# Optimization experiments

Measured on AMD Instinct MI355X. Metric: run time of the kernel, lower is better.

Reference implementation:

```python
import jax, jax.numpy as jnp
import numpy as np

NUM_ITER = 5
NUM_SLOTS = 16
INPUT_SIZE = 256
EPS = 1e-8
TAU = 1.0
B, N = 8, 16384


def setup_inputs() -> dict:
    key = jax.random.key(0)
    k1, k2 = jax.random.split(key)
    inputs = jax.random.normal(k1, (B, N, INPUT_SIZE), dtype=jnp.float32)
    # xavier_uniform for a (1, K, D) tensor (torch fan_in=K*D, fan_out=D)
    limit = float(np.sqrt(6.0 / (NUM_SLOTS * INPUT_SIZE + INPUT_SIZE)))
    slot_logits = jax.random.uniform(k2, (1, NUM_SLOTS, INPUT_SIZE),
                                     minval=-limit, maxval=limit, dtype=jnp.float32)
    mixing_coefficients = jnp.full((1, NUM_SLOTS), 1.0 / NUM_SLOTS, dtype=jnp.float32)
    return {"inputs": inputs, "slot_logits": slot_logits,
            "mixing_coefficients": mixing_coefficients}


def reference(inputs, slot_logits, mixing_coefficients):
    Bn, Nn, D = inputs.shape
    theta = jnp.broadcast_to(slot_logits, (Bn, NUM_SLOTS, D))       # (B,K,D)
    pi = jnp.broadcast_to(mixing_coefficients, (Bn, NUM_SLOTS))     # (B,K)
    p = jax.nn.softmax(inputs, axis=-1)                             # (B,N,D), loop-invariant
    for _ in range(NUM_ITER):
        log_q = jax.nn.log_softmax(theta, axis=-1)                  # (B,K,D)
        logits = jnp.einsum('bnd,bkd->bnk', p, log_q)               # (B,N,K)
        logits = logits + jnp.log(pi + EPS)[:, None, :]
        gamma = jax.nn.softmax(logits, axis=-1)                     # (B,N,K)
        pi = gamma.mean(axis=1)                                     # (B,K)
        gamma_sum = gamma.sum(axis=1) + EPS                         # (B,K)
        numerator = jnp.einsum('bnk,bnd->bkd', gamma, inputs)       # (B,K,D)
        theta = numerator / gamma_sum[:, :, None]
    g = jax.random.gumbel(jax.random.key(1), theta.shape, dtype=theta.dtype)
    slots = jax.nn.softmax((theta + g) / TAU, axis=-1)              # (B,K,D)
    return slots
```

## Files before the change

### kernel.cpp

```cpp
#include <hip/hip_runtime.h>
#include <cstdint>
#include <cstddef>

#define BN 8
#define NN 16384
#define DD 256
#define KK 16
#define NITER 5
#define EPSV 1e-8f
#define LOG256 5.545177444479562f
#define PSTR 260
#define TPB 8
#define GG 32

typedef float f32x4 __attribute__((ext_vector_type(4)));
typedef long  i64v;

__device__ __forceinline__ float frcp(float x){ return __builtin_amdgcn_rcpf(x); }
__device__ __forceinline__ float wmax(float v){
  #pragma unroll
  for (int m = 32; m >= 1; m >>= 1) v = fmaxf(v, __shfl_xor(v, m, 64));
  return v;
}
__device__ __forceinline__ float wsum(float v){
  #pragma unroll
  for (int m = 32; m >= 1; m >>= 1) v += __shfl_xor(v, m, 64);
  return v;
}
__device__ __forceinline__ uint32_t pk4_fp8(float a, float b, float c, float d){
  int w = __builtin_amdgcn_cvt_pk_fp8_f32(a, b, 0, false);
  w = __builtin_amdgcn_cvt_pk_fp8_f32(c, d, w, true);
  return (uint32_t)w;
}
__device__ __forceinline__ uint32_t f2bf(float f){
  uint32_t u = __float_as_uint(f);
  return (u + 0x7fffu + ((u >> 16) & 1u)) >> 16;
}
__device__ __forceinline__ uint32_t pk2bf(float a, float b){
  return f2bf(a) | (f2bf(b) << 16);
}
__device__ __forceinline__ float bf2f(uint32_t h){ return __uint_as_float(h << 16); }

__global__ __launch_bounds__(256, 2) void k_prep6(const float* __restrict__ x,
                                                  uint2* __restrict__ pbf8,
                                                  uint2* __restrict__ xbf8,
                                                  float* __restrict__ invs){
  __shared__ float xs[2][32 * PSTR];
  const int b = blockIdx.y;
  const int Sbase = blockIdx.x * TPB;
  const int tid = threadIdx.x;
  const int wave = tid >> 6, lane = tid & 63;
  const float* xb = x + (size_t)b * NN * DD;

  auto stage = [&](int S, int buf){
    #pragma unroll
    for (int r = 0; r < 8; ++r){
      int row = wave * 8 + r;
      const float* gp = xb + ((size_t)S * 32 + row) * DD + lane * 4;
      float* lp = &xs[buf][row * PSTR];
      __builtin_amdgcn_global_load_lds(
          (const __attribute__((address_space(1))) unsigned int*)gp,
          (__attribute__((address_space(3))) unsigned int*)lp, 16, 0, 0);
    }
  };

  stage(Sbase, 0);
  for (int it = 0; it < TPB; ++it){
    const int S = Sbase + it;
    const int cur = it & 1;
    asm volatile("s_waitcnt vmcnt(0)" ::: "memory");
    __builtin_amdgcn_sched_barrier(0);
    __syncthreads();
    if (it + 1 < TPB) stage(S + 1, cur ^ 1);

    {
      int row = 8 * wave + (lane & 7);
      const float* pr = &xs[cur][row * PSTR + (lane >> 3) * 32];
      float a = 0.f;
      #pragma unroll
      for (int i = 0; i < 8; ++i){
        float4 v = *(const float4*)&pr[4 * i];
        a += __expf(v.x) + __expf(v.y) + __expf(v.z) + __expf(v.w);
      }
      a += __shfl_xor(a, 8, 64);
      a += __shfl_xor(a, 16, 64);
      a += __shfl_xor(a, 32, 64);
      if (lane < 8) invs[(size_t)b * NN + S * 32 + 8 * wave + lane] = frcp(a);
    }

    #pragma unroll
    for (int i = 0; i < 4; ++i){
      int p = wave * 4 + i; int c = p >> 3, s = p & 7;
      int rho = lane & 15;
      int n = 8 * (rho >> 2) + 4 * c + (rho & 3);
      int d = 32 * s + 8 * (lane >> 4);
      float4 v0 = *(const float4*)&xs[cur][n * PSTR + d];
      float4 v1 = *(const float4*)&xs[cur][n * PSTR + d + 4];
      uint2 o;
      o.x = pk4_fp8(__expf(v0.x), __expf(v0.y), __expf(v0.z), __expf(v0.w));
      o.y = pk4_fp8(__expf(v1.x), __expf(v1.y), __expf(v1.z), __expf(v1.w));
      pbf8[(((size_t)b * 1024 + (size_t)S * 2 + c) * 8 + s) * 64 + lane] = o;
    }
    #pragma unroll
    for (int i = 0; i < 4; ++i){
      int dt = wave * 4 + i;
      int col = dt * 16 + (lane & 15);
      int g2 = lane >> 4;
      float v[8];
      #pragma unroll
      for (int j = 0; j < 8; ++j) v[j] = xs[cur][(8 * g2 + j) * PSTR + col];
      uint2 o;
      o.x = pk4_fp8(v[0], v[1], v[2], v[3]);
      o.y = pk4_fp8(v[4], v[5], v[6], v[7]);
      xbf8[(((size_t)b * 512 + S) * 16 + dt) * 64 + lane] = o;
    }
    __syncthreads();
  }
}

__global__ __launch_bounds__(256) void k_init6(const float* __restrict__ slot_logits,
                                               const float* __restrict__ mix,
                                               uint8_t* __restrict__ lqf8,
                                               float* __restrict__ logpi){
  int w    = blockIdx.x * 4 + (threadIdx.x >> 6);
  int lane = threadIdx.x & 63;
  int b = w >> 4, k = w & 15;
  const float4* sl = (const float4*)(slot_logits + (size_t)k * DD);
  float4 t = sl[lane];
  float m = wmax(fmaxf(fmaxf(t.x, t.y), fmaxf(t.z, t.w)));
  float s = wsum(__expf(t.x-m) + __expf(t.y-m) + __expf(t.z-m) + __expf(t.w-m));
  float L = m + __logf(s) - LOG256;
  int d0 = lane * 4;
  int ss = d0 >> 5;
  int l2 = (((d0 & 31) >> 3) << 4) + k;
  int jb = d0 & 7;
  uint32_t wv = pk4_fp8(t.x - L, t.y - L, t.z - L, t.w - L);
  *(uint32_t*)(lqf8 + ((((size_t)b * 8 + ss) * 64 + l2) * 8 + jb)) = wv;
  if (lane == 0) logpi[w] = __logf(mix[k] + EPSV);
}

__global__ __launch_bounds__(256, 2) void k_em6(const uint2* __restrict__ pbf8,
                                                const uint2* __restrict__ xbf8,
                                                const uint2* __restrict__ lqf8,
                                                const float* __restrict__ logpi,
                                                const float* __restrict__ invs,
                                                uint16_t* __restrict__ pnumb,
                                                float* __restrict__ ppi){
  __shared__ float sred[KK * DD];
  __shared__ float spi2[16];
  const int b = blockIdx.y, g = blockIdx.x;
  const int tid = threadIdx.x;
  const int wave = tid >> 6, lane = tid & 63;

  i64v lq8[8];
  {
    const uint2* p = lqf8 + (size_t)b * 8 * 64 + lane;
    #pragma unroll
    for (int s = 0; s < 8; ++s){ uint2 t = p[s * 64]; lq8[s] = *(i64v*)&t; }
  }
  const float lpik = logpi[b * KK + (lane & 15)];

  f32x4 acc[16];
  #pragma unroll
  for (int dt = 0; dt < 16; ++dt) acc[dt] = (f32x4){0.f, 0.f, 0.f, 0.f};
  float piacc = 0.f;

  const int S0 = (g * 4 + wave) * 4;
  #pragma unroll
  for (int ssi = 0; ssi < 4; ++ssi){
    const int S = S0 + ssi;
    const uint2* pb = pbf8 + (((size_t)b * 1024 + (size_t)S * 2) * 8) * 64 + lane;
    const uint2* xr = xbf8 + (((size_t)b * 512 + S) * 16) * 64 + lane;

    uint2 pa[16];
    #pragma unroll
    for (int i = 0; i < 16; ++i) pa[i] = pb[(size_t)i * 64];

    float ivs[8];
    {
      const float* ib = invs + (size_t)b * NN + S * 32 + 8 * (lane >> 4);
      #pragma unroll
      for (int j = 0; j < 8; ++j) ivs[j] = ib[j];
    }

    float ga[8];
    #pragma unroll
    for (int c = 0; c < 2; ++c){
      f32x4 lc = (f32x4){0.f, 0.f, 0.f, 0.f};
      #pragma unroll
      for (int s = 0; s < 8; ++s){
        i64v a = *(i64v*)&pa[c * 8 + s];
        lc = __builtin_amdgcn_mfma_f32_16x16x32_fp8_fp8(a, lq8[s], lc, 0, 0, 0);
      }
      #pragma unroll
      for (int r2 = 0; r2 < 4; ++r2){
        float lg = fmaf(lc[r2], ivs[c * 4 + r2], lpik);
        float mx = lg;
        #pragma unroll
        for (int m = 1; m <= 8; m <<= 1) mx = fmaxf(mx, __shfl_xor(mx, m, 64));
        float e = __expf(lg - mx);
        float s2 = e;
        #pragma unroll
        for (int m = 1; m <= 8; m <<= 1) s2 += __shfl_xor(s2, m, 64);
        ga[c * 4 + r2] = e * frcp(s2);
      }
    }
    uint2 gp;
    gp.x = pk4_fp8(ga[0], ga[1], ga[2], ga[3]);
    gp.y = pk4_fp8(ga[4], ga[5], ga[6], ga[7]);
    piacc += __builtin_amdgcn_cvt_f32_fp8((int)gp.x, 0)
           + __builtin_amdgcn_cvt_f32_fp8((int)gp.x, 1)
           + __builtin_amdgcn_cvt_f32_fp8((int)gp.x, 2)
           + __builtin_amdgcn_cvt_f32_fp8((int)gp.x, 3)
           + __builtin_amdgcn_cvt_f32_fp8((int)gp.y, 0)
           + __builtin_amdgcn_cvt_f32_fp8((int)gp.y, 1)
           + __builtin_amdgcn_cvt_f32_fp8((int)gp.y, 2)
           + __builtin_amdgcn_cvt_f32_fp8((int)gp.y, 3);
    i64v gA = *(i64v*)&gp;
    #pragma unroll
    for (int dt = 0; dt < 16; ++dt){
      uint2 xv = xr[(size_t)dt * 64];
      acc[dt] = __builtin_amdgcn_mfma_f32_16x16x32_fp8_fp8(gA, *(i64v*)&xv,
                                                           acc[dt], 0, 0, 0);
    }
  }

  float pk = piacc;
  pk += __shfl_xor(pk, 16, 64);
  pk += __shfl_xor(pk, 32, 64);
  __syncthreads();
  if (wave == 0){
    #pragma unroll
    for (int dt = 0; dt < 16; ++dt)
      #pragma unroll
      for (int r2 = 0; r2 < 4; ++r2)
        sred[(4 * (lane >> 4) + r2) * DD + dt * 16 + (lane & 15)] = acc[dt][r2];
    if (lane < 16) spi2[lane] = pk;
  }
  __syncthreads();
  for (int w = 1; w < 4; ++w){
    if (wave == w){
      #pragma unroll
      for (int dt = 0; dt < 16; ++dt)
        #pragma unroll
        for (int r2 = 0; r2 < 4; ++r2)
          sred[(4 * (lane >> 4) + r2) * DD + dt * 16 + (lane & 15)] += acc[dt][r2];
      if (lane < 16) spi2[lane] += pk;
    }
    __syncthreads();
  }
  uint32_t* dst = (uint32_t*)(pnumb + (size_t)(b * GG + g) * KK * DD);
  #pragma unroll
  for (int j = 0; j < 8; ++j){
    float a = sred[tid * 2 + j * 512];
    float c = sred[tid * 2 + 1 + j * 512];
    dst[tid + j * 256] = pk2bf(a, c);
  }
  if (tid < 16) ppi[(size_t)(b * GG + g) * KK + tid] = spi2[tid];
}

__global__ __launch_bounds__(64) void k_reduce6(const uint16_t* __restrict__ pnumb,
                                                const float* __restrict__ ppi,
                                                float* __restrict__ theta,
                                                uint8_t* __restrict__ lqf8,
                                                float* __restrict__ logpi){
  int w = blockIdx.x;
  int lane = threadIdx.x;
  int b = w >> 4, k = w & 15;
  float4 sum = make_float4(0.f, 0.f, 0.f, 0.f);
  #pragma unroll 4
  for (int g = 0; g < GG; ++g){
    const uint2* p = (const uint2*)(pnumb +
        ((size_t)(b * GG + g) * KK + k) * DD + lane * 4);
    uint2 v = *p;
    sum.x += bf2f(v.x & 0xffffu); sum.y += bf2f(v.x >> 16);
    sum.z += bf2f(v.y & 0xffffu); sum.w += bf2f(v.y >> 16);
  }
  float ps = 0.f;
  for (int g = lane; g < GG; g += 64) ps += ppi[((size_t)b * GG + g) * KK + k];
  ps = wsum(ps);
  float inv = frcp(ps + EPSV);
  float4 th = make_float4(sum.x * inv, sum.y * inv, sum.z * inv, sum.w * inv);
  ((float4*)(theta + (size_t)w * DD))[lane] = th;
  float m = wmax(fmaxf(fmaxf(th.x, th.y), fmaxf(th.z, th.w)));
  float s = wsum(__expf(th.x-m) + __expf(th.y-m) + __expf(th.z-m) + __expf(th.w-m));
  float L = m + __logf(s) - LOG256;
  int d0 = lane * 4;
  int ss = d0 >> 5;
  int l2 = (((d0 & 31) >> 3) << 4) + k;
  int jb = d0 & 7;
  uint32_t wv = pk4_fp8(th.x - L, th.y - L, th.z - L, th.w - L);
  *(uint32_t*)(lqf8 + ((((size_t)b * 8 + ss) * 64 + l2) * 8 + jb)) = wv;
  if (lane == 0) logpi[w] = __logf(ps * (1.0f / NN) + EPSV);
}

__device__ __forceinline__ uint32_t rotl32(uint32_t x, int r){ return (x << r) | (x >> (32 - r)); }
__device__ __forceinline__ void tf2x32(uint32_t k0, uint32_t k1, uint32_t c0, uint32_t c1,
                                       uint32_t& o0, uint32_t& o1){
  uint32_t ks0 = k0, ks1 = k1, ks2 = 0x1BD11BDAu ^ k0 ^ k1;
  uint32_t x0 = c0 + ks0, x1 = c1 + ks1;
  #define RND(r) { x0 += x1; x1 = rotl32(x1, r); x1 ^= x0; }
  RND(13) RND(15) RND(26) RND(6)   x0 += ks1; x1 += ks2 + 1u;
  RND(17) RND(29) RND(16) RND(24)  x0 += ks2; x1 += ks0 + 2u;
  RND(13) RND(15) RND(26) RND(6)   x0 += ks0; x1 += ks1 + 3u;
  RND(17) RND(29) RND(16) RND(24)  x0 += ks1; x1 += ks2 + 4u;
  RND(13) RND(15) RND(26) RND(6)   x0 += ks2; x1 += ks0 + 5u;
  #undef RND
  o0 = x0; o1 = x1;
}

__global__ __launch_bounds__(256) void k_final(const float* __restrict__ theta,
                                               float* __restrict__ out){
  int w    = blockIdx.x * 4 + (threadIdx.x >> 6);
  int lane = threadIdx.x & 63;
  float4 th = ((const float4*)(theta + (size_t)w * DD))[lane];
  int i0 = w * DD + lane * 4;
  float gv[4];
  #pragma unroll
  for (int j = 0; j < 4; ++j){
    uint32_t i = (uint32_t)(i0 + j);
    uint32_t o0, o1;
    tf2x32(0u, 1u, 0u, i, o0, o1);
    uint32_t bits = o0 ^ o1;
    float f = __uint_as_float((bits >> 9) | 0x3f800000u) - 1.0f;
    const float TINY = 1.17549435e-38f;
    float u = fmaxf(f + TINY, TINY);
    gv[j] = -logf(-logf(u));
  }
  float4 y = make_float4(th.x + gv[0], th.y + gv[1], th.z + gv[2], th.w + gv[3]);
  float m = wmax(fmaxf(fmaxf(y.x, y.y), fmaxf(y.z, y.w)));
  float4 e = make_float4(__expf(y.x-m), __expf(y.y-m), __expf(y.z-m), __expf(y.w-m));
  float s = wsum(e.x + e.y + e.z + e.w);
  float inv = 1.0f / s;
  ((float4*)(out + (size_t)w * DD))[lane] =
      make_float4(e.x*inv, e.y*inv, e.z*inv, e.w*inv);
}

__global__ __launch_bounds__(256) void k_fill(float* __restrict__ out, float v){
  out[blockIdx.x * 256 + threadIdx.x] = v;
}

extern "C" void kernel_launch(void* const* d_in, const int* in_sizes, int n_in,
                              void* d_out, int out_size, void* d_ws, size_t ws_size,
                              hipStream_t stream){
  const float* x    = (const float*)d_in[0];
  const float* sl   = (const float*)d_in[1];
  const float* mix  = (const float*)d_in[2];
  float* out = (float*)d_out;
  char* ws = (char*)d_ws;

  const size_t SZ_PBF  = 33554432ull;
  const size_t SZ_XBF  = 33554432ull;
  const size_t SZ_LQF  = 32768ull;
  const size_t SZ_INV  = (size_t)BN*NN*4;
  const size_t SZ_TH   = (size_t)BN*KK*DD*4;
  const size_t SZ_LP   = 512ull;
  const size_t SZ_PNUM = (size_t)BN*GG*KK*DD*2;
  const size_t SZ_PPI  = (size_t)BN*GG*KK*4;
  size_t need = SZ_PBF + SZ_XBF + SZ_LQF + SZ_INV + SZ_TH + SZ_LP + SZ_PNUM + SZ_PPI;

  if (ws_size < need){
    k_fill<<<(BN*KK*DD)/256, 256, 0, stream>>>(out, -9.0f);
    return;
  }
  size_t o = 0;
  uint2*    pbf8  = (uint2*)(ws + o);     o += SZ_PBF;
  uint2*    xbf8  = (uint2*)(ws + o);     o += SZ_XBF;
  uint8_t*  lqf8  = (uint8_t*)(ws + o);   o += SZ_LQF;
  float*    invs  = (float*)(ws + o);     o += SZ_INV;
  float*    theta = (float*)(ws + o);     o += SZ_TH;
  float*    logpi = (float*)(ws + o);     o += SZ_LP;
  uint16_t* pnumb = (uint16_t*)(ws + o);  o += SZ_PNUM;
  float*    ppi   = (float*)(ws + o);

  k_prep6<<<dim3(512 / TPB, BN), 256, 0, stream>>>(x, pbf8, xbf8, invs);
  k_init6<<<(BN*KK)/4, 256, 0, stream>>>(sl, mix, lqf8, logpi);
  for (int it = 0; it < NITER; ++it){
    k_em6    <<<dim3(GG, BN), 256, 0, stream>>>(pbf8, xbf8, (const uint2*)lqf8,
                                                logpi, invs, pnumb, ppi);
    k_reduce6<<<BN*KK, 64, 0, stream>>>(pnumb, ppi, theta, lqf8, logpi);
  }
  k_final<<<(BN*KK)/4, 256, 0, stream>>>(theta, out);
}
```

Before: 157.4 us.

## Fuse all EM stages into one persistent kernel with global atomic barriers

Replaces the chain of prep, init, per-iteration EM and reduce, and final launches with a single persistent kernel of 256 blocks that runs every stage in turn, separated by a software grid barrier built on an atomic counter. The goal is to remove the launch overhead and inter-kernel gaps of about a dozen small launches. In exchange, each block now does two prep tiles in sequence, the reduce and final stages leave most blocks idle, and correctness relies on all 256 blocks being co-resident. Spin-waiting on one atomic counter adds barrier latency, and an extra memset launch is needed to clear the counter.

```diff
diff --git a/kernel.cpp b/kernel.cpp
--- a/kernel.cpp
+++ b/kernel.cpp
@@ -41,41 +41,34 @@
 }
 __device__ __forceinline__ float bf2f(uint32_t h){ return __uint_as_float(h << 16); }
 
-__global__ __launch_bounds__(256, 2) void k_prep6(const float* __restrict__ x,
-                                                  uint2* __restrict__ pbf8,
-                                                  uint2* __restrict__ xbf8,
-                                                  float* __restrict__ invs){
-  __shared__ float xs[2][32 * PSTR];
-  const int b = blockIdx.y;
-  const int Sbase = blockIdx.x * TPB;
-  const int tid = threadIdx.x;
-  const int wave = tid >> 6, lane = tid & 63;
+
+__device__ __forceinline__ void dev_prep(const float* __restrict__ x,
+    uint2* __restrict__ pbf8, uint2* __restrict__ xbf8, float* __restrict__ invs,
+    int b, int Sbase, float* xs0, float* xs1, int wave, int lane){
   const float* xb = x + (size_t)b * NN * DD;
-
+  float* bufs[2] = {xs0, xs1};
   auto stage = [&](int S, int buf){
     #pragma unroll
     for (int r = 0; r < 8; ++r){
       int row = wave * 8 + r;
       const float* gp = xb + ((size_t)S * 32 + row) * DD + lane * 4;
-      float* lp = &xs[buf][row * PSTR];
+      float* lp = bufs[buf] + row * PSTR;
       __builtin_amdgcn_global_load_lds(
           (const __attribute__((address_space(1))) unsigned int*)gp,
           (__attribute__((address_space(3))) unsigned int*)lp, 16, 0, 0);
     }
   };
-
   stage(Sbase, 0);
   for (int it = 0; it < TPB; ++it){
     const int S = Sbase + it;
-    const int cur = it & 1;
+    float* xc = bufs[it & 1];
     asm volatile("s_waitcnt vmcnt(0)" ::: "memory");
     __builtin_amdgcn_sched_barrier(0);
     __syncthreads();
-    if (it + 1 < TPB) stage(S + 1, cur ^ 1);
-
+    if (it + 1 < TPB) stage(S + 1, (it & 1) ^ 1);
     {
       int row = 8 * wave + (lane & 7);
-      const float* pr = &xs[cur][row * PSTR + (lane >> 3) * 32];
+      const float* pr = xc + row * PSTR + (lane >> 3) * 32;
       float a = 0.f;
       #pragma unroll
       for (int i = 0; i < 8; ++i){
@@ -87,15 +80,14 @@
       a += __shfl_xor(a, 32, 64);
       if (lane < 8) invs[(size_t)b * NN + S * 32 + 8 * wave + lane] = frcp(a);
     }
-
     #pragma unroll
     for (int i = 0; i < 4; ++i){
       int p = wave * 4 + i; int c = p >> 3, s = p & 7;
       int rho = lane & 15;
       int n = 8 * (rho >> 2) + 4 * c + (rho & 3);
       int d = 32 * s + 8 * (lane >> 4);
-      float4 v0 = *(const float4*)&xs[cur][n * PSTR + d];
-      float4 v1 = *(const float4*)&xs[cur][n * PSTR + d + 4];
+      float4 v0 = *(const float4*)(xc + n * PSTR + d);
+      float4 v1 = *(const float4*)(xc + n * PSTR + d + 4);
       uint2 o;
       o.x = pk4_fp8(__expf(v0.x), __expf(v0.y), __expf(v0.z), __expf(v0.w));
       o.y = pk4_fp8(__expf(v1.x), __expf(v1.y), __expf(v1.z), __expf(v1.w));
@@ -108,7 +100,7 @@
       int g2 = lane >> 4;
       float v[8];
       #pragma unroll
-      for (int j = 0; j < 8; ++j) v[j] = xs[cur][(8 * g2 + j) * PSTR + col];
+      for (int j = 0; j < 8; ++j) v[j] = xc[(8 * g2 + j) * PSTR + col];
       uint2 o;
       o.x = pk4_fp8(v[0], v[1], v[2], v[3]);
       o.y = pk4_fp8(v[4], v[5], v[6], v[7]);
@@ -118,12 +110,9 @@
   }
 }
 
-__global__ __launch_bounds__(256) void k_init6(const float* __restrict__ slot_logits,
-                                               const float* __restrict__ mix,
-                                               uint8_t* __restrict__ lqf8,
-                                               float* __restrict__ logpi){
-  int w    = blockIdx.x * 4 + (threadIdx.x >> 6);
-  int lane = threadIdx.x & 63;
+__device__ __forceinline__ void dev_init(const float* __restrict__ slot_logits,
+    const float* __restrict__ mix, uint8_t* __restrict__ lqf8,
+    float* __restrict__ logpi, int w, int lane){
   int b = w >> 4, k = w & 15;
   const float4* sl = (const float4*)(slot_logits + (size_t)k * DD);
   float4 t = sl[lane];
@@ -139,22 +128,14 @@
   if (lane == 0) logpi[w] = __logf(mix[k] + EPSV);
 }
 
-__global__ __launch_bounds__(256, 2) void k_em6(const uint2* __restrict__ pbf8,
-                                                const uint2* __restrict__ xbf8,
-                                                const uint2* __restrict__ lqf8,
-                                                const float* __restrict__ logpi,
-                                                const float* __restrict__ invs,
-                                                uint16_t* __restrict__ pnumb,
-                                                float* __restrict__ ppi){
-  __shared__ float sred[KK * DD];
-  __shared__ float spi2[16];
-  const int b = blockIdx.y, g = blockIdx.x;
-  const int tid = threadIdx.x;
-  const int wave = tid >> 6, lane = tid & 63;
-
+__device__ __forceinline__ void dev_em(const uint2* __restrict__ pbf8,
+    const uint2* __restrict__ xbf8, const uint2* __restrict__ lqf8v,
+    const float* __restrict__ logpi, const float* __restrict__ invs,
+    uint16_t* __restrict__ pnumb, float* __restrict__ ppi,
+    int b, int g, float* sred, float* spi2, int wave, int lane, int tid){
   i64v lq8[8];
   {
-    const uint2* p = lqf8 + (size_t)b * 8 * 64 + lane;
+    const uint2* p = lqf8v + (size_t)b * 8 * 64 + lane;
     #pragma unroll
     for (int s = 0; s < 8; ++s){ uint2 t = p[s * 64]; lq8[s] = *(i64v*)&t; }
   }
@@ -171,18 +152,15 @@
     const int S = S0 + ssi;
     const uint2* pb = pbf8 + (((size_t)b * 1024 + (size_t)S * 2) * 8) * 64 + lane;
     const uint2* xr = xbf8 + (((size_t)b * 512 + S) * 16) * 64 + lane;
-
     uint2 pa[16];
     #pragma unroll
     for (int i = 0; i < 16; ++i) pa[i] = pb[(size_t)i * 64];
-
     float ivs[8];
     {
       const float* ib = invs + (size_t)b * NN + S * 32 + 8 * (lane >> 4);
       #pragma unroll
       for (int j = 0; j < 8; ++j) ivs[j] = ib[j];
     }
-
     float ga[8];
     #pragma unroll
     for (int c = 0; c < 2; ++c){
@@ -259,13 +237,9 @@
   if (tid < 16) ppi[(size_t)(b * GG + g) * KK + tid] = spi2[tid];
 }
 
-__global__ __launch_bounds__(64) void k_reduce6(const uint16_t* __restrict__ pnumb,
-                                                const float* __restrict__ ppi,
-                                                float* __restrict__ theta,
-                                                uint8_t* __restrict__ lqf8,
-                                                float* __restrict__ logpi){
-  int w = blockIdx.x;
-  int lane = threadIdx.x;
+__device__ __forceinline__ void dev_reduce(const uint16_t* __restrict__ pnumb,
+    const float* __restrict__ ppi, float* __restrict__ theta,
+    uint8_t* __restrict__ lqf8, float* __restrict__ logpi, int w, int lane){
   int b = w >> 4, k = w & 15;
   float4 sum = make_float4(0.f, 0.f, 0.f, 0.f);
   #pragma unroll 4
@@ -309,10 +283,8 @@
   o0 = x0; o1 = x1;
 }
 
-__global__ __launch_bounds__(256) void k_final(const float* __restrict__ theta,
-                                               float* __restrict__ out){
-  int w    = blockIdx.x * 4 + (threadIdx.x >> 6);
-  int lane = threadIdx.x & 63;
+__device__ __forceinline__ void dev_final(const float* __restrict__ theta,
+                                          float* __restrict__ out, int w, int lane){
   float4 th = ((const float4*)(theta + (size_t)w * DD))[lane];
   int i0 = w * DD + lane * 4;
   float gv[4];
@@ -336,6 +308,81 @@
       make_float4(e.x*inv, e.y*inv, e.z*inv, e.w*inv);
 }
 
+__device__ __forceinline__ void gbar(uint32_t* bar, uint32_t goal){
+  __syncthreads();
+  if (threadIdx.x == 0){
+    __threadfence();
+    atomicAdd(bar, 1u);
+    while (atomicAdd(bar, 0u) < goal) __builtin_amdgcn_s_sleep(4);
+  }
+  __syncthreads();
+  __threadfence();
+}
+
+__global__ __launch_bounds__(256, 2) void k_fused(
+    const float* __restrict__ x, const float* __restrict__ sl,
+    const float* __restrict__ mix,
+    uint2* __restrict__ pbf8, uint2* __restrict__ xbf8,
+    uint8_t* __restrict__ lqf8, float* __restrict__ invs,
+    float* __restrict__ theta, float* __restrict__ logpi,
+    uint16_t* __restrict__ pnumb, float* __restrict__ ppi,
+    float* __restrict__ out, uint32_t* __restrict__ bar){
+  __shared__ float xs[2][32 * PSTR];
+  __shared__ float spi2[16];
+  const int bid = blockIdx.x;
+  const int tid = threadIdx.x;
+  const int wave = tid >> 6, lane = tid & 63;
+  uint32_t nb = 0;
+
+  for (int ui = 0; ui < 2; ++ui){
+    int u = bid + ui * 256;
+    dev_prep(x, pbf8, xbf8, invs, u >> 6, (u & 63) * TPB,
+             &xs[0][0], &xs[1][0], wave, lane);
+  }
+  if (bid < 32) dev_init(sl, mix, lqf8, logpi, bid * 4 + wave, lane);
+  gbar(bar, 256u * (++nb));
+
+  for (int it = 0; it < NITER; ++it){
+    dev_em(pbf8, xbf8, (const uint2*)lqf8, logpi, invs, pnumb, ppi,
+           bid >> 5, bid & 31, &xs[0][0], spi2, wave, lane, tid);
+    gbar(bar, 256u * (++nb));
+    if (bid < 128 && wave == 0)
+      dev_reduce(pnumb, ppi, theta, lqf8, logpi, bid, lane);
+    gbar(bar, 256u * (++nb));
+  }
+  if (bid < 32) dev_final(theta, out, bid * 4 + wave, lane);
+}
+
+__global__ __launch_bounds__(256, 2) void k_prep6(const float* __restrict__ x,
+    uint2* __restrict__ pbf8, uint2* __restrict__ xbf8, float* __restrict__ invs){
+  __shared__ float xs[2][32 * PSTR];
+  dev_prep(x, pbf8, xbf8, invs, blockIdx.y, blockIdx.x * TPB,
+           &xs[0][0], &xs[1][0], threadIdx.x >> 6, threadIdx.x & 63);
+}
+__global__ __launch_bounds__(256) void k_init6(const float* __restrict__ sl,
+    const float* __restrict__ mix, uint8_t* __restrict__ lqf8,
+    float* __restrict__ logpi){
+  dev_init(sl, mix, lqf8, logpi, blockIdx.x * 4 + (threadIdx.x >> 6),
+           threadIdx.x & 63);
+}
+__global__ __launch_bounds__(256, 2) void k_em6(const uint2* __restrict__ pbf8,
+    const uint2* __restrict__ xbf8, const uint2* __restrict__ lqf8v,
+    const float* __restrict__ logpi, const float* __restrict__ invs,
+    uint16_t* __restrict__ pnumb, float* __restrict__ ppi){
+  __shared__ float sred[KK * DD];
+  __shared__ float spi2[16];
+  dev_em(pbf8, xbf8, lqf8v, logpi, invs, pnumb, ppi, blockIdx.y, blockIdx.x,
+         sred, spi2, threadIdx.x >> 6, threadIdx.x & 63, threadIdx.x);
+}
+__global__ __launch_bounds__(64) void k_reduce6(const uint16_t* __restrict__ pnumb,
+    const float* __restrict__ ppi, float* __restrict__ theta,
+    uint8_t* __restrict__ lqf8, float* __restrict__ logpi){
+  dev_reduce(pnumb, ppi, theta, lqf8, logpi, blockIdx.x, threadIdx.x);
+}
+__global__ __launch_bounds__(256) void k_final(const float* __restrict__ theta,
+                                               float* __restrict__ out){
+  dev_final(theta, out, blockIdx.x * 4 + (threadIdx.x >> 6), threadIdx.x & 63);
+}
 __global__ __launch_bounds__(256) void k_fill(float* __restrict__ out, float v){
   out[blockIdx.x * 256 + threadIdx.x] = v;
 }
@@ -357,7 +404,9 @@
   const size_t SZ_LP   = 512ull;
   const size_t SZ_PNUM = (size_t)BN*GG*KK*DD*2;
   const size_t SZ_PPI  = (size_t)BN*GG*KK*4;
-  size_t need = SZ_PBF + SZ_XBF + SZ_LQF + SZ_INV + SZ_TH + SZ_LP + SZ_PNUM + SZ_PPI;
+  const size_t SZ_BAR  = 64ull;
+  size_t need = SZ_PBF + SZ_XBF + SZ_LQF + SZ_INV + SZ_TH + SZ_LP
+              + SZ_PNUM + SZ_PPI + SZ_BAR;
 
   if (ws_size < need){
     k_fill<<<(BN*KK*DD)/256, 256, 0, stream>>>(out, -9.0f);
@@ -371,14 +420,10 @@
   float*    theta = (float*)(ws + o);     o += SZ_TH;
   float*    logpi = (float*)(ws + o);     o += SZ_LP;
   uint16_t* pnumb = (uint16_t*)(ws + o);  o += SZ_PNUM;
-  float*    ppi   = (float*)(ws + o);
-
-  k_prep6<<<dim3(512 / TPB, BN), 256, 0, stream>>>(x, pbf8, xbf8, invs);
-  k_init6<<<(BN*KK)/4, 256, 0, stream>>>(sl, mix, lqf8, logpi);
-  for (int it = 0; it < NITER; ++it){
-    k_em6    <<<dim3(GG, BN), 256, 0, stream>>>(pbf8, xbf8, (const uint2*)lqf8,
-                                                logpi, invs, pnumb, ppi);
-    k_reduce6<<<BN*KK, 64, 0, stream>>>(pnumb, ppi, theta, lqf8, logpi);
-  }
-  k_final<<<(BN*KK)/4, 256, 0, stream>>>(theta, out);
-}
+  float*    ppi   = (float*)(ws + o);     o += SZ_PPI;
+  uint32_t* bar   = (uint32_t*)(ws + o);
+
+  hipMemsetAsync(bar, 0, SZ_BAR, stream);
+  k_fused<<<256, 256, 0, stream>>>(x, sl, mix, pbf8, xbf8, lqf8, invs,
+                                   theta, logpi, pnumb, ppi, out, bar);
+}
```

Result: slower. 557.4 us (+254.2%).
